# Optimization experiments

Hardware: AMD Instinct MI355X
Metric: run time of the kernel (lower is better)

The kernel has to match this reference:

```python
import jax, jax.numpy as jnp
import numpy as np

NUM_HEADS = 16


def setup_inputs() -> dict:
    key = jax.random.key(0)
    k1, k2, k3 = jax.random.split(key, 3)
    B, N, C = 4, 2048, 1024
    x = jax.random.normal(k1, (B, N, C), dtype=jnp.float32)
    qkv_w = jax.random.normal(k2, (3 * C, C), dtype=jnp.float32) * (C ** -0.5)
    proj_w = jax.random.normal(k3, (C, C), dtype=jnp.float32) * (C ** -0.5)
    proj_b = jnp.zeros((C,), dtype=jnp.float32)
    return {"x": x, "qkv_w": qkv_w, "proj_w": proj_w, "proj_b": proj_b, "len_t": 256}


def reference(x, qkv_w, proj_w, proj_b, len_t):
    B, N, C = x.shape
    H = NUM_HEADS
    hd = C // H
    scale = hd ** -0.5
    # qkv: [B, N, 3C] -> [3, B, H, N, hd]
    qkv = (x @ qkv_w.T).reshape(B, N, 3, H, hd).transpose(2, 0, 3, 1, 4)
    q, k, v = qkv[0], qkv[1], qkv[2]
    q_s = q[:, :, len_t:]                      # [B, H, N-len_t, hd] partial queries
    attn = jnp.einsum('bhqd,bhkd->bhqk', q_s, k) * scale
    attn = jax.nn.softmax(attn, axis=-1)       # [B, H, N-len_t, N]
    x_s = jnp.einsum('bhqk,bhkd->bhqd', attn, v)
    x_s = x_s.transpose(0, 2, 1, 3).reshape(B, N - len_t, C)
    x_t = x[:, :len_t]                         # template tokens pass through
    x_out = jnp.concatenate((x_t, x_s), axis=1)
    return x_out @ proj_w.T + proj_b
```

## Files before the change

### kernel.cpp

```cpp
#include <hip/hip_runtime.h>
#include <stdint.h>

typedef unsigned short u16;
typedef __attribute__((ext_vector_type(4))) short short4v;
typedef __attribute__((ext_vector_type(8))) short short8;
typedef __attribute__((ext_vector_type(4))) float floatx4;
typedef __attribute__((ext_vector_type(4))) unsigned short u16x4;

typedef __attribute__((address_space(1))) const void* gas_ptr;
typedef __attribute__((address_space(3))) void* las_ptr;

__device__ __forceinline__ void async16(const void* g, void* l) {
    __builtin_amdgcn_global_load_lds((gas_ptr)g, (las_ptr)l, 16, 0, 0);
}

__device__ __forceinline__ u16 f2bf(float f) {
    union { float f; unsigned int u; } v; v.f = f;
    unsigned int r = v.u + 0x7fffu + ((v.u >> 16) & 1u);
    return (u16)(r >> 16);
}

__device__ __forceinline__ int pk_bf16(float a, float b) {
    return (int)((unsigned int)f2bf(a) | ((unsigned int)f2bf(b) << 16));
}

__device__ __forceinline__ int pk2t(float a, float b) {
    union { float f; unsigned int u; } ua, ub;
    ua.f = a; ub.f = b;
    return (int)__builtin_amdgcn_perm(ub.u, ua.u, 0x07060302u);
}

__global__ void cvt_w_kernel(const float* __restrict__ src, u16* __restrict__ dst) {
    int i = blockIdx.x * 256 + threadIdx.x;
    float4 f = reinterpret_cast<const float4*>(src)[i];
    u16x4 o;
    o.x = f2bf(f.x); o.y = f2bf(f.y); o.z = f2bf(f.z); o.w = f2bf(f.w);
    reinterpret_cast<u16x4*>(dst)[i] = o;
}

__global__ void cvt_x_kernel(const float* __restrict__ x, u16* __restrict__ xb,
                             u16* __restrict__ xout) {
    int i = blockIdx.x * 256 + threadIdx.x;
    float4 f = reinterpret_cast<const float4*>(x)[i];
    u16x4 o;
    o.x = f2bf(f.x); o.y = f2bf(f.y); o.z = f2bf(f.z); o.w = f2bf(f.w);
    reinterpret_cast<u16x4*>(xb)[i] = o;
    int m = (i * 4) >> 10;
    if ((m & 2047) < 256) reinterpret_cast<u16x4*>(xout)[i] = o;
}

template<int MODE>
__global__ void __launch_bounds__(256, 2)
gemm_nt(const u16* __restrict__ A, const u16* __restrict__ B,
        u16* __restrict__ q_out, u16* __restrict__ k_out, u16* __restrict__ vt_out,
        float* __restrict__ f_out, const float* __restrict__ bias, int K) {
    __shared__ u16 As[3][128 * 32];
    __shared__ u16 Bs[3][128 * 32];
    const int tid  = threadIdx.x;
    const int lane = tid & 63;
    const int w    = tid >> 6;
    const int row0 = blockIdx.x * 128;
    const int col0 = blockIdx.y * 128;
    const int wm   = (w >> 1) * 64;
    const int wn   = (w & 1) * 64;

    floatx4 acc[4][4] = {};

#define STAGE_G(buf, kelem)                                                     \
    do {                                                                        \
        _Pragma("unroll")                                                       \
        for (int i = 0; i < 2; ++i) {                                           \
            int pb = w * 128 + i * 64;                                          \
            int p  = pb + lane;                                                 \
            int r  = p >> 2;                                                    \
            int c  = (p & 3) ^ ((r >> 1) & 3);                                  \
            async16(A + (size_t)(row0 + r) * K + ((kelem) + c * 8),             \
                    (char*)&As[buf][0] + p * 16);                               \
            async16(B + (size_t)(col0 + r) * K + ((kelem) + c * 8),             \
                    (char*)&Bs[buf][0] + p * 16);                               \
        }                                                                       \
    } while (0)

    STAGE_G(0, 0);
    STAGE_G(1, 32);
    const int nk = K >> 5;

    int cur = 0;
    int nx2 = 2;
    for (int kt = 0; kt < nk; ++kt) {
        if (kt + 1 < nk) {
            asm volatile("s_waitcnt vmcnt(4)" ::: "memory");
        } else {
            asm volatile("s_waitcnt vmcnt(0)" ::: "memory");
        }
        __builtin_amdgcn_s_barrier();
        __builtin_amdgcn_sched_barrier(0);
        if (kt + 2 < nk) STAGE_G(nx2, (kt + 2) << 5);

        const u16* as = &As[cur][0];
        const u16* bs = &Bs[cur][0];
        short8 af[4], bf_[4];
#pragma unroll
        for (int t = 0; t < 4; ++t) {
            int ar = wm + t * 16 + (lane & 15);
            int ca = (lane >> 4) ^ ((ar >> 1) & 3);
            af[t]  = *(const short8*)(as + ar * 32 + ca * 8);
            int br = wn + t * 16 + (lane & 15);
            int cb = (lane >> 4) ^ ((br >> 1) & 3);
            bf_[t] = *(const short8*)(bs + br * 32 + cb * 8);
        }
#pragma unroll
        for (int i = 0; i < 4; ++i)
#pragma unroll
            for (int j = 0; j < 4; ++j)
                acc[i][j] = __builtin_amdgcn_mfma_f32_16x16x32_bf16(af[i], bf_[j], acc[i][j], 0, 0, 0);

        cur = (cur == 2) ? 0 : cur + 1;
        nx2 = (nx2 == 2) ? 0 : nx2 + 1;
    }
#undef STAGE_G

#pragma unroll
    for (int i = 0; i < 4; ++i) {
#pragma unroll
        for (int j = 0; j < 4; ++j) {
            int gr0 = row0 + wm + i * 16 + ((lane >> 4) << 2);
            int gc  = col0 + wn + j * 16 + (lane & 15);
            if (MODE == 0) {
                int which = gc >> 10;
                int cl = gc & 1023;
                int h = cl >> 6, d = cl & 63;
                int b = gr0 >> 11, n0 = gr0 & 2047;
                int bh = b * 16 + h;
                if (which == 2) {
                    u16x4 pk;
                    pk.x = f2bf(acc[i][j][0]); pk.y = f2bf(acc[i][j][1]);
                    pk.z = f2bf(acc[i][j][2]); pk.w = f2bf(acc[i][j][3]);
                    size_t off = (size_t)bh * 131072
                               + (((size_t)(n0 >> 5) * 4 + (d >> 4)) * 64
                                  + ((n0 >> 3) & 3) * 16 + (d & 15)) * 8 + (n0 & 4);
                    *reinterpret_cast<u16x4*>(vt_out + off) = pk;
                } else {
                    u16* dst = (which == 0) ? q_out : k_out;
                    float sc = (which == 0) ? 0.18033688f : 1.0f;
#pragma unroll
                    for (int r = 0; r < 4; ++r)
                        dst[((size_t)bh * 2048 + n0 + r) * 64 + d] = f2bf(acc[i][j][r] * sc);
                }
            } else {
                float bv = bias[gc];
#pragma unroll
                for (int r = 0; r < 4; ++r)
                    f_out[(size_t)(gr0 + r) * 1024 + gc] = acc[i][j][r] + bv;
            }
        }
    }
}

__global__ void __launch_bounds__(256, 3)
flash_attn(const u16* __restrict__ Qg, const u16* __restrict__ Kg,
           const u16* __restrict__ Vf, u16* __restrict__ xout) {
    __shared__ u16 Ks[2][64 * 64];
    __shared__ u16 Vs[2][8 * 512];
    const int lane = threadIdx.x & 63;
    const int w    = threadIdx.x >> 6;
    const int bh   = blockIdx.x & 63;
    const int qt   = blockIdx.x >> 6;
    const int q0   = 256 + qt * 128 + w * 32;
    const size_t kvbase = (size_t)bh * 2048 * 64;

    const int m = lane & 15;
    const int g = lane >> 4;

    short8 qf[2][2];
#pragma unroll
    for (int qs = 0; qs < 2; ++qs) {
        const u16* p = Qg + kvbase + (size_t)(q0 + qs * 16 + m) * 64 + g * 8;
        qf[qs][0] = *(const short8*)(p);
        qf[qs][1] = *(const short8*)(p + 32);
    }

    const u16* vg = Vf + (size_t)bh * 131072;

    const int p0 = w * 64 + lane;
    const int tid = threadIdx.x;
#define STAGE_KV(buf, kt)                                                       \
    {                                                                           \
        _Pragma("unroll")                                                       \
        for (int i = 0; i < 2; ++i) {                                           \
            int p = i * 256 + p0;                                               \
            int r = p >> 3;                                                     \
            int c = (p & 7) ^ ((((r >> 3) & 1) << 2) | (r & 3));                \
            async16(Kg + kvbase + (size_t)((kt) * 64 + r) * 64 + c * 8,         \
                    (char*)&Ks[buf][0] + p * 16);                               \
        }                                                                       \
        _Pragma("unroll")                                                       \
        for (int i = 0; i < 2; ++i) {                                           \
            int p = i * 256 + tid;                                              \
            async16(vg + (size_t)((kt) * 8 + (p >> 6)) * 512 + (p & 63) * 8,    \
                    (char*)&Vs[buf][0] + p * 16);                               \
        }                                                                       \
    }

    STAGE_KV(0, 0);

    const floatx4 ZROW = {-32.f, -32.f, -32.f, -32.f};
    short8 ones1;
#pragma unroll
    for (int i = 0; i < 8; ++i) ones1[i] = (short)0x3F80;

    floatx4 lacc[2] = {};
    floatx4 o[2][4] = {};

    const int fm = ((m >> 2) & 1) * 4 + (m & 3);

    for (int kt = 0; kt < 32; ++kt) {
        __syncthreads();
        if (kt + 1 < 32) STAGE_KV((kt + 1) & 1, kt + 1);

        const u16* kbuf = &Ks[kt & 1][0];
        const u16* vbuf = &Vs[kt & 1][0];
#pragma unroll
        for (int b32 = 0; b32 < 2; ++b32) {
            short8 vfr[4];
#pragma unroll
            for (int i = 0; i < 4; ++i)
                vfr[i] = *(const short8*)(vbuf + ((b32 * 4 + i) * 64 + lane) * 8);

            floatx4 sT[2][2];
#pragma unroll
            for (int t = 0; t < 2; ++t) {
                int r = b32 * 32 + (m >> 2) * 8 + t * 4 + (m & 3);
                short8 k0 = *(const short8*)(kbuf + r * 64 + ((g)     ^ fm) * 8);
                short8 k1 = *(const short8*)(kbuf + r * 64 + ((4 + g) ^ fm) * 8);
                __builtin_amdgcn_s_setprio(1);
#pragma unroll
                for (int qs = 0; qs < 2; ++qs) {
                    floatx4 z = __builtin_amdgcn_mfma_f32_16x16x32_bf16(k0, qf[qs][0], ZROW, 0, 0, 0);
                    sT[qs][t] = __builtin_amdgcn_mfma_f32_16x16x32_bf16(k1, qf[qs][1], z, 0, 0, 0);
                }
                __builtin_amdgcn_s_setprio(0);
            }

#pragma unroll
            for (int qs = 0; qs < 2; ++qs) {
                float p[8];
#pragma unroll
                for (int t = 0; t < 2; ++t)
#pragma unroll
                    for (int r = 0; r < 4; ++r)
                        p[t * 4 + r] = __builtin_amdgcn_exp2f(sT[qs][t][r]);
                union { int i4[4]; short8 s8; } u;
                u.i4[0] = pk2t(p[0], p[1]);
                u.i4[1] = pk2t(p[2], p[3]);
                u.i4[2] = pk2t(p[4], p[5]);
                u.i4[3] = pk2t(p[6], p[7]);
                __builtin_amdgcn_s_setprio(1);
#pragma unroll
                for (int i = 0; i < 4; ++i)
                    o[qs][i] = __builtin_amdgcn_mfma_f32_16x16x32_bf16(vfr[i], u.s8, o[qs][i], 0, 0, 0);
                lacc[qs] = __builtin_amdgcn_mfma_f32_16x16x32_bf16(ones1, u.s8, lacc[qs], 0, 0, 0);
                __builtin_amdgcn_s_setprio(0);
            }
        }
    }

    const int b = bh >> 4, h = bh & 15;
#pragma unroll
    for (int qs = 0; qs < 2; ++qs) {
        const float inv = 1.f / lacc[qs][0];

        const int n = q0 + qs * 16 + m;
        u16* dst = xout + (size_t)(b * 2048 + n) * 1024 + h * 64 + (g << 2);
#pragma unroll
        for (int i = 0; i < 4; ++i) {
            union { int i2[2]; u16x4 s4; } u;
            u.i2[0] = pk_bf16(o[qs][i][0] * inv, o[qs][i][1] * inv);
            u.i2[1] = pk_bf16(o[qs][i][2] * inv, o[qs][i][3] * inv);
            *reinterpret_cast<u16x4*>(dst + i * 16) = u.s4;
        }
    }
#undef STAGE_KV
}

extern "C" void kernel_launch(void* const* d_in, const int* in_sizes, int n_in,
                              void* d_out, int out_size, void* d_ws, size_t ws_size,
                              hipStream_t stream) {
    const float* x      = (const float*)d_in[0];
    const float* qkv_w  = (const float*)d_in[1];
    const float* proj_w = (const float*)d_in[2];
    const float* proj_b = (const float*)d_in[3];

    char* ws = (char*)d_ws;
    u16* xb    = (u16*)(ws);
    u16* xout  = (u16*)(ws + ((size_t)16 << 20));
    u16* wqkv  = (u16*)(ws + ((size_t)32 << 20));
    u16* wproj = (u16*)(ws + ((size_t)38 << 20));
    u16* Qb    = (u16*)(ws + ((size_t)40 << 20));
    u16* Kb    = (u16*)(ws + ((size_t)56 << 20));
    u16* Vfb   = (u16*)(ws + ((size_t)72 << 20));

    cvt_x_kernel<<<8192, 256, 0, stream>>>(x, xb, xout);
    cvt_w_kernel<<<3072, 256, 0, stream>>>(qkv_w, wqkv);
    cvt_w_kernel<<<1024, 256, 0, stream>>>(proj_w, wproj);
    gemm_nt<0><<<dim3(64, 24), 256, 0, stream>>>(xb, wqkv, Qb, Kb, Vfb, nullptr, nullptr, 1024);
    flash_attn<<<896, 256, 0, stream>>>(Qb, Kb, Vfb, xout);
    gemm_nt<1><<<dim3(64, 8), 256, 0, stream>>>(xout, wproj, nullptr, nullptr, nullptr,
                                                (float*)d_out, proj_b, 1024);
}
```

Before: 254.6 us.

## Add dedicated 256x192-tile QKV GEMM kernel with 8 waves and split staging

Replaces the generic 128x128 gemm_nt for the QKV projection with a specialized kernel that uses 512 threads, a 256x192 output tile, XOR-swizzled LDS layout and a 3-stage async load pipeline. Each k-step is split into two halves, with A and B prefetches interleaved between MFMA batches and s_setprio raised around them. The larger tile is meant to raise arithmetic intensity and cut global/LDS traffic per FLOP. The grid shrinks to 512 blocks, and LDS use per block grows to about 84KB. That may limit occupancy and leave the last wave of blocks unbalanced.

```diff
diff --git a/kernel.cpp b/kernel.cpp
--- a/kernel.cpp
+++ b/kernel.cpp
@@ -49,10 +49,131 @@
     if ((m & 2047) < 256) reinterpret_cast<u16x4*>(xout)[i] = o;
 }
 
+__global__ void __launch_bounds__(512, 2)
+gemm_qkv(const u16* __restrict__ A, const u16* __restrict__ B,
+         u16* __restrict__ q_out, u16* __restrict__ k_out, u16* __restrict__ vt_out) {
+    __shared__ u16 As[3][256 * 32];
+    __shared__ u16 Bs[3][192 * 32];
+    const int tid  = threadIdx.x;
+    const int lane = tid & 63;
+    const int w    = tid >> 6;
+    const int wr   = w >> 2;
+    const int wc   = w & 3;
+    const int row0 = blockIdx.x * 256;
+    const int col0 = blockIdx.y * 192;
+    const int m    = lane & 15;
+    const int g    = lane >> 4;
+
+    floatx4 acc[8][3] = {};
+
+#define STAGE_A8(buf, kelem)                                                    \
+    do {                                                                        \
+        _Pragma("unroll")                                                       \
+        for (int i = 0; i < 2; ++i) {                                           \
+            int p = tid + i * 512;                                              \
+            int r = p >> 2;                                                     \
+            int c = (p & 3) ^ ((r >> 1) & 3);                                   \
+            async16(A + (size_t)(row0 + r) * 1024 + ((kelem) + c * 8),          \
+                    (char*)&As[buf][0] + p * 16);                               \
+        }                                                                       \
+    } while (0)
+
+#define STAGE_B8(buf, kelem)                                                    \
+    do {                                                                        \
+        _Pragma("unroll")                                                       \
+        for (int i = 0; i < 2; ++i) {                                           \
+            int p = (i == 0) ? tid : (tid + 256);                               \
+            int r = p >> 2;                                                     \
+            int c = (p & 3) ^ ((r >> 1) & 3);                                   \
+            async16(B + (size_t)(col0 + r) * 1024 + ((kelem) + c * 8),          \
+                    (char*)&Bs[buf][0] + p * 16);                               \
+        }                                                                       \
+    } while (0)
+
+    STAGE_A8(0, 0);  STAGE_B8(0, 0);
+    STAGE_A8(1, 32); STAGE_B8(1, 32);
+
+    int cur = 0, nx2 = 2;
+    for (int kt = 0; kt < 32; ++kt) {
+        if (kt < 31) asm volatile("s_waitcnt vmcnt(4)" ::: "memory");
+        else         asm volatile("s_waitcnt vmcnt(0)" ::: "memory");
+        __builtin_amdgcn_s_barrier();
+
+        const u16* as = &As[cur][0];
+        const u16* bs = &Bs[cur][0];
+        short8 af[8], bf[3];
+#pragma unroll
+        for (int j = 0; j < 3; ++j) {
+            int br = wc * 48 + j * 16 + m;
+            bf[j] = *(const short8*)(bs + br * 32 + (g ^ ((br >> 1) & 3)) * 8);
+        }
+#pragma unroll
+        for (int i = 0; i < 4; ++i) {
+            int ar = wr * 128 + i * 16 + m;
+            af[i] = *(const short8*)(as + ar * 32 + (g ^ ((ar >> 1) & 3)) * 8);
+        }
+        if (kt + 2 < 32) STAGE_A8(nx2, (kt + 2) * 32);
+        __builtin_amdgcn_s_setprio(1);
+#pragma unroll
+        for (int i = 0; i < 4; ++i)
+#pragma unroll
+            for (int j = 0; j < 3; ++j)
+                acc[i][j] = __builtin_amdgcn_mfma_f32_16x16x32_bf16(af[i], bf[j], acc[i][j], 0, 0, 0);
+        __builtin_amdgcn_s_setprio(0);
+        __builtin_amdgcn_s_barrier();
+#pragma unroll
+        for (int i = 4; i < 8; ++i) {
+            int ar = wr * 128 + i * 16 + m;
+            af[i] = *(const short8*)(as + ar * 32 + (g ^ ((ar >> 1) & 3)) * 8);
+        }
+        if (kt + 2 < 32) STAGE_B8(nx2, (kt + 2) * 32);
+        __builtin_amdgcn_s_setprio(1);
+#pragma unroll
+        for (int i = 4; i < 8; ++i)
+#pragma unroll
+            for (int j = 0; j < 3; ++j)
+                acc[i][j] = __builtin_amdgcn_mfma_f32_16x16x32_bf16(af[i], bf[j], acc[i][j], 0, 0, 0);
+        __builtin_amdgcn_s_setprio(0);
+
+        cur = (cur == 2) ? 0 : cur + 1;
+        nx2 = (nx2 == 2) ? 0 : nx2 + 1;
+    }
+#undef STAGE_A8
+#undef STAGE_B8
+
+#pragma unroll
+    for (int i = 0; i < 8; ++i) {
+#pragma unroll
+        for (int j = 0; j < 3; ++j) {
+            int gr0 = row0 + wr * 128 + i * 16 + (g << 2);
+            int gc  = col0 + wc * 48 + j * 16 + m;
+            int which = gc >> 10;
+            int cl = gc & 1023;
+            int h = cl >> 6, d = cl & 63;
+            int b = gr0 >> 11, n0 = gr0 & 2047;
+            int bh = b * 16 + h;
+            if (which == 2) {
+                u16x4 pk;
+                pk.x = f2bf(acc[i][j][0]); pk.y = f2bf(acc[i][j][1]);
+                pk.z = f2bf(acc[i][j][2]); pk.w = f2bf(acc[i][j][3]);
+                size_t off = (size_t)bh * 131072
+                           + (((size_t)(n0 >> 5) * 4 + (d >> 4)) * 64
+                              + ((n0 >> 3) & 3) * 16 + (d & 15)) * 8 + (n0 & 4);
+                *reinterpret_cast<u16x4*>(vt_out + off) = pk;
+            } else {
+                u16* dst = (which == 0) ? q_out : k_out;
+                float sc = (which == 0) ? 0.18033688f : 1.0f;
+#pragma unroll
+                for (int r = 0; r < 4; ++r)
+                    dst[((size_t)bh * 2048 + n0 + r) * 64 + d] = f2bf(acc[i][j][r] * sc);
+            }
+        }
+    }
+}
+
 template<int MODE>
 __global__ void __launch_bounds__(256, 2)
 gemm_nt(const u16* __restrict__ A, const u16* __restrict__ B,
-        u16* __restrict__ q_out, u16* __restrict__ k_out, u16* __restrict__ vt_out,
         float* __restrict__ f_out, const float* __restrict__ bias, int K) {
     __shared__ u16 As[3][128 * 32];
     __shared__ u16 Bs[3][128 * 32];
@@ -126,33 +247,10 @@
         for (int j = 0; j < 4; ++j) {
             int gr0 = row0 + wm + i * 16 + ((lane >> 4) << 2);
             int gc  = col0 + wn + j * 16 + (lane & 15);
-            if (MODE == 0) {
-                int which = gc >> 10;
-                int cl = gc & 1023;
-                int h = cl >> 6, d = cl & 63;
-                int b = gr0 >> 11, n0 = gr0 & 2047;
-                int bh = b * 16 + h;
-                if (which == 2) {
-                    u16x4 pk;
-                    pk.x = f2bf(acc[i][j][0]); pk.y = f2bf(acc[i][j][1]);
-                    pk.z = f2bf(acc[i][j][2]); pk.w = f2bf(acc[i][j][3]);
-                    size_t off = (size_t)bh * 131072
-                               + (((size_t)(n0 >> 5) * 4 + (d >> 4)) * 64
-                                  + ((n0 >> 3) & 3) * 16 + (d & 15)) * 8 + (n0 & 4);
-                    *reinterpret_cast<u16x4*>(vt_out + off) = pk;
-                } else {
-                    u16* dst = (which == 0) ? q_out : k_out;
-                    float sc = (which == 0) ? 0.18033688f : 1.0f;
-#pragma unroll
-                    for (int r = 0; r < 4; ++r)
-                        dst[((size_t)bh * 2048 + n0 + r) * 64 + d] = f2bf(acc[i][j][r] * sc);
-                }
-            } else {
-                float bv = bias[gc];
-#pragma unroll
-                for (int r = 0; r < 4; ++r)
-                    f_out[(size_t)(gr0 + r) * 1024 + gc] = acc[i][j][r] + bv;
-            }
+            float bv = bias[gc];
+#pragma unroll
+            for (int r = 0; r < 4; ++r)
+                f_out[(size_t)(gr0 + r) * 1024 + gc] = acc[i][j][r] + bv;
         }
     }
 }
@@ -303,8 +401,7 @@
     cvt_x_kernel<<<8192, 256, 0, stream>>>(x, xb, xout);
     cvt_w_kernel<<<3072, 256, 0, stream>>>(qkv_w, wqkv);
     cvt_w_kernel<<<1024, 256, 0, stream>>>(proj_w, wproj);
-    gemm_nt<0><<<dim3(64, 24), 256, 0, stream>>>(xb, wqkv, Qb, Kb, Vfb, nullptr, nullptr, 1024);
+    gemm_qkv<<<dim3(32, 16), 512, 0, stream>>>(xb, wqkv, Qb, Kb, Vfb);
     flash_attn<<<896, 256, 0, stream>>>(Qb, Kb, Vfb, xout);
-    gemm_nt<1><<<dim3(64, 8), 256, 0, stream>>>(xout, wproj, nullptr, nullptr, nullptr,
-                                                (float*)d_out, proj_b, 1024);
-}
+    gemm_nt<1><<<dim3(64, 8), 256, 0, stream>>>(xout, wproj, (float*)d_out, proj_b, 1024);
+}
```

After: 255.9 us. Within noise of the previous version (+0.5%).
